# Kernel optimization log

Hardware: AMD Instinct MI355X
Metric: run time of the kernel (lower is better)

The kernel has to match this reference:

```python
import jax, jax.numpy as jnp
import numpy as np

DIM = 1024
NH = 16
HD = DIM // NH  # 64
B, S = 4, 2048
EPS = 1e-5


def layer_norm(x, g, b):
    mu = jnp.mean(x, axis=-1, keepdims=True)
    var = jnp.mean(jnp.square(x - mu), axis=-1, keepdims=True)
    return (x - mu) * jax.lax.rsqrt(var + EPS) * g + b


def setup_inputs() -> dict:
    key = jax.random.key(0)
    ks = jax.random.split(key, 12)
    std = 0.02
    return {
        "x": jax.random.normal(ks[0], (B, S, DIM), jnp.float32),
        "ln1_g": jnp.ones((DIM,), jnp.float32),
        "ln1_b": jnp.zeros((DIM,), jnp.float32),
        # per-head Q/K/V linears stacked over heads: [NH, DIM, HD]
        "Wq": jax.random.normal(ks[1], (NH, DIM, HD), jnp.float32) * std,
        "bq": jnp.zeros((NH, HD), jnp.float32),
        "Wk": jax.random.normal(ks[2], (NH, DIM, HD), jnp.float32) * std,
        "bk": jnp.zeros((NH, HD), jnp.float32),
        "Wv": jax.random.normal(ks[3], (NH, DIM, HD), jnp.float32) * std,
        "bv": jnp.zeros((NH, HD), jnp.float32),
        "ln2_g": jnp.ones((DIM,), jnp.float32),
        "ln2_b": jnp.zeros((DIM,), jnp.float32),
        # FC block: LayerNorm -> Linear(dim,4dim) -> GELU -> Linear(4dim,dim) -> GELU
        "fcln_g": jnp.ones((DIM,), jnp.float32),
        "fcln_b": jnp.zeros((DIM,), jnp.float32),
        "W1": jax.random.normal(ks[4], (DIM, 4 * DIM), jnp.float32) * std,
        "b1": jnp.zeros((4 * DIM,), jnp.float32),
        "W2": jax.random.normal(ks[5], (4 * DIM, DIM), jnp.float32) * std,
        "b2": jnp.zeros((DIM,), jnp.float32),
    }


def reference(x, ln1_g, ln1_b, Wq, bq, Wk, bk, Wv, bv,
              ln2_g, ln2_b, fcln_g, fcln_b, W1, b1, W2, b2):
    # --- MHA branch: x + concat_h(head_h(ln1(x))) ---
    h = layer_norm(x, ln1_g, ln1_b)                       # [B,S,D]
    q = jnp.einsum('bsd,hdk->bhsk', h, Wq) + bq[None, :, None, :]
    k = jnp.einsum('bsd,hdk->bhsk', h, Wk) + bk[None, :, None, :]
    v = jnp.einsum('bsd,hdk->bhsk', h, Wv) + bv[None, :, None, :]
    scores = jnp.einsum('bhsk,bhtk->bhst', q, k) / jnp.sqrt(jnp.float32(HD))
    causal = jnp.tril(jnp.ones((S, S), bool))
    scores = jnp.where(causal[None, None], scores, jnp.float32(-1e9))
    attn = jax.nn.softmax(scores, axis=-1)                # [B,NH,S,S]
    o = jnp.einsum('bhst,bhtk->bhsk', attn, v)            # [B,NH,S,HD]
    o = o.transpose(0, 2, 1, 3).reshape(B, S, DIM)        # concat heads
    x = x + o
    # --- FC branch: x + GELU(GELU(LN(ln2(x)) @ W1) @ W2) ---
    h2 = layer_norm(x, ln2_g, ln2_b)
    h2 = layer_norm(h2, fcln_g, fcln_b)
    h2 = jax.nn.gelu(h2 @ W1 + b1, approximate=False)
    h2 = jax.nn.gelu(h2 @ W2 + b2, approximate=False)
    return x + h2
```

## Files before the change

### kernel.cpp

```cpp
#include <hip/hip_runtime.h>
#include <math.h>

#define DIMD 1024
#define NHD  16
#define HDD  64
#define BBB  4
#define SSS  2048
#define MMM  (BBB*SSS)

typedef __bf16 bf16;
typedef __bf16 bf16x8 __attribute__((ext_vector_type(8)));
typedef __bf16 bf16x4 __attribute__((ext_vector_type(4)));
typedef float  f32x4  __attribute__((ext_vector_type(4)));


__device__ __forceinline__ void gld16(const void* g, void* l) {
  __builtin_amdgcn_global_load_lds((const __attribute__((address_space(1))) void*)g,
                                   (__attribute__((address_space(3))) void*)l,
                                   16, 0, 0);
}

__device__ __forceinline__ f32x4 mfma_bf16(bf16x8 a, bf16x8 b, f32x4 c) {
  return __builtin_amdgcn_mfma_f32_16x16x32_bf16(a, b, c, 0, 0, 0);
}

__device__ __forceinline__ float gelu_f(float x) {
  const float u2 = 1.5957691216057308f * x * (1.0f + 0.044715f * x * x);
  const float e = __expf(u2);
  float r;
  asm("v_rcp_f32 %0, %1" : "=v"(r) : "v"(e + 1.0f));
  return x * (1.0f - r);
}

__device__ __forceinline__ void blockReduce2(float& s, float& s2, float* red) {
  #pragma unroll
  for (int m = 1; m < 64; m <<= 1) {
    s  += __shfl_xor(s,  m);
    s2 += __shfl_xor(s2, m);
  }
  const int wave = threadIdx.x >> 6, lane = threadIdx.x & 63;
  __syncthreads();
  if (lane == 0) { red[wave*2] = s; red[wave*2+1] = s2; }
  __syncthreads();
  s  = red[0] + red[2] + red[4] + red[6];
  s2 = red[1] + red[3] + red[5] + red[7];
}

#define SBAR() do { __builtin_amdgcn_sched_barrier(0); __builtin_amdgcn_s_barrier(); \
                    __builtin_amdgcn_sched_barrier(0); } while (0)
#define LGKM0() do { asm volatile("s_waitcnt lgkmcnt(0)" ::: "memory"); \
                     __builtin_amdgcn_sched_barrier(0); } while (0)
#define LGKMC(n) do { asm volatile("s_waitcnt lgkmcnt(" #n ")" ::: "memory"); \
                      __builtin_amdgcn_sched_barrier(0); } while (0)
#define VMC(n)  do { asm volatile("s_waitcnt vmcnt(" #n ")" ::: "memory"); \
                     __builtin_amdgcn_sched_barrier(0); } while (0)


__global__ __launch_bounds__(256)
void transpose_k(const float* __restrict__ in, bf16* __restrict__ out, int R, int C) {
  __shared__ float tile[32][33];
  const int z = blockIdx.z;
  in  += (size_t)z * R * C;
  out += (size_t)z * R * C;
  const int r0 = blockIdx.x * 32, c0 = blockIdx.y * 32;
  const int tx = threadIdx.x, ty = threadIdx.y;
  #pragma unroll
  for (int k = 0; k < 4; ++k)
    tile[ty + k*8][tx] = in[(size_t)(r0 + ty + k*8) * C + c0 + tx];
  __syncthreads();
  #pragma unroll
  for (int k = 0; k < 4; ++k)
    out[(size_t)(c0 + ty + k*8) * R + r0 + tx] = (bf16)tile[tx][ty + k*8];
}


__global__ __launch_bounds__(256)
void transpose_qkv_k(const float* __restrict__ Wq, const float* __restrict__ Wk,
                     const float* __restrict__ Wv, bf16* __restrict__ out) {
  __shared__ float tile[32][33];
  const int z = blockIdx.z;
  const int which = z >> 4, zh = z & 15;
  const float* in = (which == 0 ? Wq : (which == 1 ? Wk : Wv)) + (size_t)zh * 1024 * 64;
  bf16* op = out + (size_t)z * 64 * 1024;
  const int r0 = blockIdx.x * 32, c0 = blockIdx.y * 32;
  const int tx = threadIdx.x, ty = threadIdx.y;
  #pragma unroll
  for (int k = 0; k < 4; ++k)
    tile[ty + k*8][tx] = in[(size_t)(r0 + ty + k*8) * 64 + c0 + tx];
  __syncthreads();
  #pragma unroll
  for (int k = 0; k < 4; ++k)
    op[(size_t)(c0 + ty + k*8) * 1024 + r0 + tx] = (bf16)tile[tx][ty + k*8];
}


__global__ __launch_bounds__(256)
void transpose_v_k(const bf16* __restrict__ in, bf16* __restrict__ out) {
  __shared__ bf16 t[64*72];
  const int z = blockIdx.y;
  const int s0 = blockIdx.x * 64;
  const bf16* ip = in + (size_t)z * SSS * HDD + (size_t)s0 * HDD;
  bf16* op = out + (size_t)z * SSS * HDD + s0;
  const int tid = threadIdx.x;
  #pragma unroll
  for (int p = 0; p < 2; ++p) {
    const int r = p*32 + (tid >> 3);
    const int c = (tid & 7) * 8;
    const int cs = c ^ (((r >> 3) & 7) << 3);
    *(bf16x8*)&t[r*72 + cs] = *(const bf16x8*)&ip[(size_t)r * HDD + c];
  }
  __syncthreads();
  #pragma unroll
  for (int p = 0; p < 2; ++p) {
    const int hd = p*32 + (tid >> 3);
    const int c0 = (tid & 7) * 8;
    bf16x8 v;
    #pragma unroll
    for (int j = 0; j < 8; ++j) {
      const int r = c0 + j;
      v[j] = t[r*72 + (hd ^ (((r >> 3) & 7) << 3))];
    }
    *(bf16x8*)&op[(size_t)hd * SSS + c0] = v;
  }
}


__global__ __launch_bounds__(256)
void ln1_k(const float* __restrict__ x, const float* __restrict__ g,
           const float* __restrict__ b, bf16* __restrict__ out) {
  __shared__ float red[8];
  const int row = blockIdx.x, t = threadIdx.x;
  const float4 v = ((const float4*)(x + (size_t)row * DIMD))[t];
  float s  = v.x + v.y + v.z + v.w;
  float s2 = v.x*v.x + v.y*v.y + v.z*v.z + v.w*v.w;
  blockReduce2(s, s2, red);
  const float mu   = s * (1.0f / DIMD);
  const float var  = s2 * (1.0f / DIMD) - mu * mu;
  const float rstd = rsqrtf(var + 1e-5f);
  const float4 gv = ((const float4*)g)[t];
  const float4 bv = ((const float4*)b)[t];
  bf16x4 o;
  o[0] = (bf16)((v.x - mu) * rstd * gv.x + bv.x);
  o[1] = (bf16)((v.y - mu) * rstd * gv.y + bv.y);
  o[2] = (bf16)((v.z - mu) * rstd * gv.z + bv.z);
  o[3] = (bf16)((v.w - mu) * rstd * gv.w + bv.w);
  *(bf16x4*)(out + (size_t)row * DIMD + t*4) = o;
}


__global__ __launch_bounds__(256)
void ln2fc_k(const float* __restrict__ x1,
             const float* __restrict__ g2, const float* __restrict__ b2,
             const float* __restrict__ g3, const float* __restrict__ b3,
             bf16* __restrict__ out) {
  __shared__ float red[8];
  const int row = blockIdx.x, t = threadIdx.x;
  const float4 v = ((const float4*)(x1 + (size_t)row * DIMD))[t];
  float s  = v.x + v.y + v.z + v.w;
  float s2 = v.x*v.x + v.y*v.y + v.z*v.z + v.w*v.w;
  blockReduce2(s, s2, red);
  float mu   = s * (1.0f / DIMD);
  float rstd = rsqrtf(s2 * (1.0f / DIMD) - mu * mu + 1e-5f);
  const float4 gv2 = ((const float4*)g2)[t];
  const float4 bv2 = ((const float4*)b2)[t];
  float y0 = (v.x - mu) * rstd * gv2.x + bv2.x;
  float y1 = (v.y - mu) * rstd * gv2.y + bv2.y;
  float y2 = (v.z - mu) * rstd * gv2.z + bv2.z;
  float y3 = (v.w - mu) * rstd * gv2.w + bv2.w;
  s  = y0 + y1 + y2 + y3;
  s2 = y0*y0 + y1*y1 + y2*y2 + y3*y3;
  blockReduce2(s, s2, red);
  mu   = s * (1.0f / DIMD);
  rstd = rsqrtf(s2 * (1.0f / DIMD) - mu * mu + 1e-5f);
  const float4 gv3 = ((const float4*)g3)[t];
  const float4 bv3 = ((const float4*)b3)[t];
  bf16x4 o;
  o[0] = (bf16)((y0 - mu) * rstd * gv3.x + bv3.x);
  o[1] = (bf16)((y1 - mu) * rstd * gv3.y + bv3.y);
  o[2] = (bf16)((y2 - mu) * rstd * gv3.z + bv3.z);
  o[3] = (bf16)((y3 - mu) * rstd * gv3.w + bv3.w);
  *(bf16x4*)(out + (size_t)row * DIMD + t*4) = o;
}


template<int MH2>
__device__ __forceinline__ void load_aH(bf16x8 (&d)[MH2][2], const bf16* base, int roff,
                                        int qv, int sw) {
  #pragma unroll
  for (int mi = 0; mi < MH2; ++mi)
    #pragma unroll
    for (int kk = 0; kk < 2; ++kk)
      d[mi][kk] = *(const bf16x8*)&base[roff + mi*1024 + (((kk<<2)+qv)^sw)*8];
}

__device__ __forceinline__ void load_b2(bf16x8 (&d)[2][2], const bf16* base, int roff,
                                        int qv, int sw) {
  #pragma unroll
  for (int nj = 0; nj < 2; ++nj)
    #pragma unroll
    for (int kk = 0; kk < 2; ++kk)
      d[nj][kk] = *(const bf16x8*)&base[roff + nj*1024 + (((kk<<2)+qv)^sw)*8];
}

template<int EPI, int MH2>
__global__ __launch_bounds__(512)
void gemm8p(const bf16* __restrict__ A, const bf16* __restrict__ Bt,
            int K, int N, int nbx,
            const float* __restrict__ bias, bf16* __restrict__ outB,
            float* __restrict__ outF,
            const float* __restrict__ bq, const float* __restrict__ bk,
            const float* __restrict__ bv) {
  constexpr int BM = 64 * MH2;
  __shared__ bf16 sA[2][BM*64];
  __shared__ bf16 sB[2][256*64];
  const int tid = threadIdx.x, wave = tid >> 6, lane = tid & 63;
  const int wm = wave >> 2, wn = wave & 3;

  const int q8 = gridDim.x >> 3;
  const int wg = (blockIdx.x & 7) * q8 + (blockIdx.x >> 3);
  const int by = wg / nbx, bx = wg - by * nbx;
  const int row0 = by * BM, col0 = bx * 256;

  const int l8 = lane >> 3, l7 = lane & 7;
  const int gsw = (l7 ^ l8) * 8;
  const int lo = lane & 15, qv = lane >> 4, sw = lane & 7;

  const bf16* Ags = A  + (size_t)(row0 + wave*8 + l8) * K + gsw;
  const bf16* Bgs = Bt + (size_t)(col0 + wave*8 + l8) * K + gsw;

  #define STAGE_A(buf, r, kt) gld16(Ags + (size_t)(r)*64*K + (kt), &sA[buf][(r)*4096 + wave*512])
  #define STAGE_B(buf, r, kt) gld16(Bgs + (size_t)(r)*64*K + (kt), &sB[buf][(r)*4096 + wave*512])

  const int fA = (wm*(32*MH2) + lo) * 64;
  const int fB = (wn*64       + lo) * 64;

  f32x4 acc[2*MH2][4] = {};
  bf16x8 aL[MH2][2], aU[MH2][2], b0[2][2], b1[2][2];
  const int NT = K >> 6;

  #pragma unroll
  for (int r = 0; r < MH2; ++r) STAGE_A(0, r, 0);
  #pragma unroll
  for (int r = 0; r < 4; ++r)   STAGE_B(0, r, 0);
  #pragma unroll
  for (int j = 0; j < MH2/2; ++j) STAGE_A(1, 2*j, 64);
  if (MH2 == 4) { VMC(2); } else { VMC(1); }
  SBAR();

  for (int t = 0; t < NT; ++t) {
    const int cur = t & 1, nxt = cur ^ 1;
    const int kt1 = (t + 1) << 6, kt2 = (t + 2) << 6;
    const bf16* cA = &sA[0][0] + cur * (BM*64);
    const bf16* cB = &sB[0][0] + cur * (256*64);

    load_aH<MH2>(aL, cA, fA, qv, sw);
    load_b2(b0, cB, fB, qv, sw);
    load_b2(b1, cB, fB + 2048, qv, sw);
    load_aH<MH2>(aU, cA, fA + MH2*1024, qv, sw);
    if (t + 1 < NT) {
      #pragma unroll
      for (int j = 0; j < MH2/2; ++j) STAGE_A(nxt, 2*j + 1, kt1);
      #pragma unroll
      for (int r = 0; r < 4; ++r)     STAGE_B(nxt, r, kt1);
    }

    if (MH2 == 4) { LGKMC(12); } else { LGKMC(8); }
    __builtin_amdgcn_s_setprio(1);
    #pragma unroll
    for (int mi = 0; mi < MH2; ++mi)
      #pragma unroll
      for (int nj = 0; nj < 2; ++nj)
        #pragma unroll
        for (int kk = 0; kk < 2; ++kk)
          acc[mi][nj] = mfma_bf16(aL[mi][kk], b0[nj][kk], acc[mi][nj]);
    __builtin_amdgcn_s_setprio(0);

    if (MH2 == 4) { LGKMC(8); } else { LGKMC(4); }
    __builtin_amdgcn_s_setprio(1);
    #pragma unroll
    for (int mi = 0; mi < MH2; ++mi)
      #pragma unroll
      for (int nj = 0; nj < 2; ++nj)
        #pragma unroll
        for (int kk = 0; kk < 2; ++kk)
          acc[mi][2+nj] = mfma_bf16(aL[mi][kk], b1[nj][kk], acc[mi][2+nj]);
    __builtin_amdgcn_s_setprio(0);

    LGKM0();
    SBAR();
    if (t + 2 < NT) {
      #pragma unroll
      for (int j = 0; j < MH2/2; ++j) STAGE_A(cur, 2*j, kt2);
    }

    __builtin_amdgcn_s_setprio(1);
    #pragma unroll
    for (int mi = 0; mi < MH2; ++mi)
      #pragma unroll
      for (int nj = 0; nj < 2; ++nj)
        #pragma unroll
        for (int kk = 0; kk < 2; ++kk)
          acc[MH2+mi][nj] = mfma_bf16(aU[mi][kk], b0[nj][kk], acc[MH2+mi][nj]);
    #pragma unroll
    for (int mi = 0; mi < MH2; ++mi)
      #pragma unroll
      for (int nj = 0; nj < 2; ++nj)
        #pragma unroll
        for (int kk = 0; kk < 2; ++kk)
          acc[MH2+mi][2+nj] = mfma_bf16(aU[mi][kk], b1[nj][kk], acc[MH2+mi][2+nj]);
    __builtin_amdgcn_s_setprio(0);

    if (t + 1 < NT) {
      if (t + 2 < NT) { if (MH2 == 4) { VMC(2); } else { VMC(1); } }
      else            { VMC(0); }
      SBAR();
    }
  }
  #undef STAGE_A
  #undef STAGE_B

  #pragma unroll
  for (int mi = 0; mi < 2*MH2; ++mi)
    #pragma unroll
    for (int ni = 0; ni < 4; ++ni)
      #pragma unroll
      for (int i = 0; i < 4; ++i) {
        const int row = row0 + wm*(32*MH2) + mi*16 + qv*4 + i;
        const int col = col0 + wn*64 + ni*16 + lo;
        float v = acc[mi][ni][i];
        if (EPI == 0) {
          const int which = col >> 10, h = (col >> 6) & 15, hd = col & 63;
          const float* bp = (which == 0) ? bq : ((which == 1) ? bk : bv);
          v += bp[h*64 + hd];
          if (which == 0) v *= 0.125f;
          const int b_ = row >> 11, s_ = row & 2047;
          const size_t dst = ((((size_t)which*BBB + b_)*NHD + h)*SSS + s_)*HDD + hd;
          outB[dst] = (bf16)v;
        } else if (EPI == 1) {
          v = gelu_f(v + bias[col]);
          outB[(size_t)row * N + col] = (bf16)v;
        } else {
          v = gelu_f(v + bias[col]);
          outF[(size_t)row * N + col] += v;
        }
      }
}


__global__ __launch_bounds__(256)
void attn_k(const bf16* __restrict__ qkv, const bf16* __restrict__ Vt,
            const float* __restrict__ x, float* __restrict__ out) {
  __shared__ bf16 sK[64*72];
  __shared__ bf16 sVt[80*72];
  __shared__ bf16 sP[128*72];
  const int bh = blockIdx.y;
  const int b = bh >> 4, h = bh & 15;
  const int tid = threadIdx.x, wave = tid >> 6, lane = tid & 63;
  const size_t plane = (size_t)BBB * NHD * SSS * HDD;
  const bf16* Qp  = qkv + ((size_t)b * NHD + h) * SSS * HDD;
  const bf16* Kp  = Qp + plane;
  const bf16* Vtp = Vt + ((size_t)b * NHD + h) * SSS * HDD;

  const int r8 = tid >> 3;
  const int c8 = (tid & 7) * 8;
  const int lo = lane & 15, qv = lane >> 4;

  for (int j = tid; j < 16*72; j += 256) sVt[64*72 + j] = (bf16)1.0f;

  for (int pass = 0; pass < 2; ++pass) {
    const int q0 = (pass == 0 ? (int)blockIdx.x : 15 - (int)blockIdx.x) * 128;

    bf16x8 aq[2][2];
    #pragma unroll
    for (int mi = 0; mi < 2; ++mi)
      #pragma unroll
      for (int kk = 0; kk < 2; ++kk)
        aq[mi][kk] = *(const bf16x8*)&Qp[(size_t)(q0 + wave*32 + mi*16 + lo) * HDD
                                         + kk*32 + qv * 8];

    f32x4 o[2][5] = {};

    bf16x8 rk0, rk1, rv0, rv1;
    rk0 = *(const bf16x8*)&Kp[(size_t)r8 * HDD + c8];
    rk1 = *(const bf16x8*)&Kp[(size_t)(32 + r8) * HDD + c8];
    rv0 = *(const bf16x8*)&Vtp[(size_t)r8 * SSS + c8];
    rv1 = *(const bf16x8*)&Vtp[(size_t)(32 + r8) * SSS + c8];

    const int nt = (q0 + 128) / 64;
    for (int t = 0; t < nt; ++t) {
      const int kv0 = t * 64;
      __syncthreads();
      *(bf16x8*)&sK[r8*72 + c8]        = rk0;
      *(bf16x8*)&sK[(32 + r8)*72 + c8] = rk1;
      *(bf16x8*)&sVt[r8*72 + c8]        = rv0;
      *(bf16x8*)&sVt[(32 + r8)*72 + c8] = rv1;
      __syncthreads();
      if (t + 1 < nt) {
        const int kn = kv0 + 64;
        rk0 = *(const bf16x8*)&Kp[(size_t)(kn + r8) * HDD + c8];
        rk1 = *(const bf16x8*)&Kp[(size_t)(kn + 32 + r8) * HDD + c8];
        rv0 = *(const bf16x8*)&Vtp[(size_t)r8 * SSS + kn + c8];
        rv1 = *(const bf16x8*)&Vtp[(size_t)(32 + r8) * SSS + kn + c8];
      }
      if (kv0 <= q0 + wave*32 + 31) {
        f32x4 s[2][4] = {};
        #pragma unroll
        for (int kk = 0; kk < 2; ++kk)
          #pragma unroll
          for (int ni = 0; ni < 4; ++ni) {
            const bf16x8 ak_ = *(const bf16x8*)&sK[(ni*16 + lo)*72 + kk*32 + qv*8];
            s[0][ni] = mfma_bf16(ak_, aq[0][kk], s[0][ni]);
            s[1][ni] = mfma_bf16(ak_, aq[1][kk], s[1][ni]);
          }
        if (kv0 + 63 > q0 + wave*32) {
          #pragma unroll
          for (int mi = 0; mi < 2; ++mi)
            #pragma unroll
            for (int ni = 0; ni < 4; ++ni)
              #pragma unroll
              for (int i = 0; i < 4; ++i) {
                const int kvg = kv0 + ni*16 + qv*4 + i;
                const int qg  = q0 + wave*32 + mi*16 + lo;
                if (kvg > qg) s[mi][ni][i] = -1e30f;
              }
        }
        #pragma unroll
        for (int mi = 0; mi < 2; ++mi)
          #pragma unroll
          for (int ni = 0; ni < 4; ++ni) {
            bf16x4 pk;
            #pragma unroll
            for (int i = 0; i < 4; ++i) pk[i] = (bf16)__expf(s[mi][ni][i]);
            *(bf16x4*)&sP[(wave*32 + mi*16 + lo)*72 + ni*16 + qv*4] = pk;
          }
        asm volatile("s_waitcnt lgkmcnt(0)" ::: "memory");
        __builtin_amdgcn_sched_barrier(0);
        #pragma unroll
        for (int ks = 0; ks < 2; ++ks) {
          bf16x8 ap[2];
          ap[0] = *(const bf16x8*)&sP[(wave*32 +      lo)*72 + ks*32 + qv*8];
          ap[1] = *(const bf16x8*)&sP[(wave*32 + 16 + lo)*72 + ks*32 + qv*8];
          #pragma unroll
          for (int hf = 0; hf < 5; ++hf) {
            const bf16x8 bv_ = *(const bf16x8*)&sVt[(hf*16 + lo)*72 + ks*32 + qv*8];
            o[0][hf] = mfma_bf16(ap[0], bv_, o[0][hf]);
            o[1][hf] = mfma_bf16(ap[1], bv_, o[1][hf]);
          }
        }
      }
    }
    #pragma unroll
    for (int mi = 0; mi < 2; ++mi) {
      float inv[4];
      #pragma unroll
      for (int i = 0; i < 4; ++i) inv[i] = 1.0f / o[mi][4][i];
      #pragma unroll
      for (int hf = 0; hf < 4; ++hf)
        #pragma unroll
        for (int i = 0; i < 4; ++i) {
          const int srow = q0 + wave*32 + mi*16 + qv*4 + i;
          const int col  = h*HDD + hf*16 + lo;
          const size_t idx = ((size_t)b * SSS + srow) * DIMD + col;
          out[idx] = x[idx] + o[mi][hf][i] * inv[i];
        }
    }
  }
}


extern "C" void kernel_launch(void* const* d_in, const int* in_sizes, int n_in,
                              void* d_out, int out_size, void* d_ws, size_t ws_size,
                              hipStream_t stream) {
  const float* x     = (const float*)d_in[0];
  const float* ln1g  = (const float*)d_in[1];
  const float* ln1b  = (const float*)d_in[2];
  const float* Wq    = (const float*)d_in[3];
  const float* bq    = (const float*)d_in[4];
  const float* Wk    = (const float*)d_in[5];
  const float* bk    = (const float*)d_in[6];
  const float* Wv    = (const float*)d_in[7];
  const float* bv    = (const float*)d_in[8];
  const float* ln2g  = (const float*)d_in[9];
  const float* ln2b  = (const float*)d_in[10];
  const float* fclng = (const float*)d_in[11];
  const float* fclnb = (const float*)d_in[12];
  const float* W1    = (const float*)d_in[13];
  const float* b1    = (const float*)d_in[14];
  const float* W2    = (const float*)d_in[15];
  const float* b2    = (const float*)d_in[16];
  float* out = (float*)d_out;

  char* ws = (char*)d_ws;
  bf16* h     = (bf16*)(ws);
  bf16* Wqkvt = (bf16*)(ws + 16777216);
  bf16* W1t   = (bf16*)(ws + 23068672);
  bf16* W2t   = (bf16*)(ws + 31457280);
  bf16* qkv   = (bf16*)(ws + 39845888);
  bf16* u     = (bf16*)(ws + 39845888);
  bf16* VtB   = h;
  const size_t plane = (size_t)BBB * NHD * SSS * HDD;

  const dim3 tb(32, 8);
  transpose_qkv_k<<<dim3(32, 2, 48), tb, 0, stream>>>(Wq, Wk, Wv, Wqkvt);
  transpose_k<<<dim3(32, 128, 1), tb, 0, stream>>>(W1, W1t, 1024, 4096);
  transpose_k<<<dim3(128, 32, 1), tb, 0, stream>>>(W2, W2t, 4096, 1024);

  ln1_k<<<MMM, 256, 0, stream>>>(x, ln1g, ln1b, h);

  gemm8p<0,2><<<dim3(768), 512, 0, stream>>>(h, Wqkvt, 1024, 3072, 12,
                                             nullptr, qkv, nullptr, bq, bk, bv);

  transpose_v_k<<<dim3(SSS/64, BBB*NHD), 256, 0, stream>>>(qkv + 2*plane, VtB);

  attn_k<<<dim3(8, BBB*NHD), 256, 0, stream>>>(qkv, VtB, x, out);

  ln2fc_k<<<MMM, 256, 0, stream>>>(out, ln2g, ln2b, fclng, fclnb, h);

  gemm8p<1,4><<<dim3(512), 512, 0, stream>>>(h, W1t, 1024, 4096, 16,
                                             b1, u, nullptr, nullptr, nullptr, nullptr);

  gemm8p<2,2><<<dim3(256), 512, 0, stream>>>(u, W2t, 4096, 1024, 4,
                                             b2, nullptr, out, nullptr, nullptr, nullptr);
}
```

Baseline: 339.0 us.

## Restructure GEMM main loop into 8-phase ping-pong schedule with finer-grained staging

Rewrites the gemm8p main loop to process two K-tiles per iteration. Each tile is split into four MFMA quadrants, and each quadrant is separated by barriers, with LDS fragment loads and global-to-LDS staging interleaved between them. B tiles are now prefetched a full stage ahead, and the global loads are spread evenly across phases. The aim is better overlap of memory traffic with MFMA work, at the cost of many more workgroup barriers. The loop also assumes NT is even.

Result: slower. 359.0 us (+5.9%).

```diff
diff --git a/kernel.cpp b/kernel.cpp
--- a/kernel.cpp
+++ b/kernel.cpp
@@ -50,8 +50,6 @@
                     __builtin_amdgcn_sched_barrier(0); } while (0)
 #define LGKM0() do { asm volatile("s_waitcnt lgkmcnt(0)" ::: "memory"); \
                      __builtin_amdgcn_sched_barrier(0); } while (0)
-#define LGKMC(n) do { asm volatile("s_waitcnt lgkmcnt(" #n ")" ::: "memory"); \
-                      __builtin_amdgcn_sched_barrier(0); } while (0)
 #define VMC(n)  do { asm volatile("s_waitcnt vmcnt(" #n ")" ::: "memory"); \
                      __builtin_amdgcn_sched_barrier(0); } while (0)
 
@@ -202,6 +200,20 @@
       d[nj][kk] = *(const bf16x8*)&base[roff + nj*1024 + (((kk<<2)+qv)^sw)*8];
 }
 
+template<int AM, int AN, int MH2>
+__device__ __forceinline__ void quad(f32x4 (&acc)[2*MH2][4], const bf16x8 (&af)[MH2][2],
+                                     const bf16x8 (&bf_)[2][2]) {
+  __builtin_amdgcn_s_setprio(1);
+  #pragma unroll
+  for (int mi = 0; mi < MH2; ++mi)
+    #pragma unroll
+    for (int nj = 0; nj < 2; ++nj)
+      #pragma unroll
+      for (int kk = 0; kk < 2; ++kk)
+        acc[AM+mi][AN+nj] = mfma_bf16(af[mi][kk], bf_[nj][kk], acc[AM+mi][AN+nj]);
+  __builtin_amdgcn_s_setprio(0);
+}
+
 template<int EPI, int MH2>
 __global__ __launch_bounds__(512)
 void gemm8p(const bf16* __restrict__ A, const bf16* __restrict__ Bt,
@@ -237,82 +249,86 @@
   f32x4 acc[2*MH2][4] = {};
   bf16x8 aL[MH2][2], aU[MH2][2], b0[2][2], b1[2][2];
   const int NT = K >> 6;
-
-  #pragma unroll
-  for (int r = 0; r < MH2; ++r) STAGE_A(0, r, 0);
-  #pragma unroll
-  for (int r = 0; r < 4; ++r)   STAGE_B(0, r, 0);
-  #pragma unroll
-  for (int j = 0; j < MH2/2; ++j) STAGE_A(1, 2*j, 64);
-  if (MH2 == 4) { VMC(2); } else { VMC(1); }
+  const int NI = NT >> 1;
+
+  const bf16* cA0 = &sA[0][0];
+  const bf16* cB0 = &sB[0][0];
+  const bf16* cA1 = &sA[1][0];
+  const bf16* cB1 = &sB[1][0];
+
+  if (MH2 == 4) {
+    STAGE_A(0,0,0); STAGE_A(0,1,0); STAGE_A(0,2,0); STAGE_A(0,3,0);
+    STAGE_B(0,0,0); STAGE_B(0,1,0); STAGE_B(0,2,0); STAGE_B(0,3,0);
+    STAGE_A(1,0,64); STAGE_A(1,2,64);
+    STAGE_B(1,0,64); STAGE_B(1,1,64); STAGE_B(1,2,64); STAGE_B(1,3,64);
+    VMC(6);
+  } else {
+    STAGE_A(0,0,0); STAGE_A(0,1,0);
+    STAGE_B(0,0,0); STAGE_B(0,1,0); STAGE_B(0,2,0); STAGE_B(0,3,0);
+    STAGE_B(1,0,64); STAGE_B(1,1,64); STAGE_B(1,2,64); STAGE_B(1,3,64);
+    VMC(4);
+  }
   SBAR();
 
-  for (int t = 0; t < NT; ++t) {
-    const int cur = t & 1, nxt = cur ^ 1;
-    const int kt1 = (t + 1) << 6, kt2 = (t + 2) << 6;
-    const bf16* cA = &sA[0][0] + cur * (BM*64);
-    const bf16* cB = &sB[0][0] + cur * (256*64);
-
-    load_aH<MH2>(aL, cA, fA, qv, sw);
-    load_b2(b0, cB, fB, qv, sw);
-    load_b2(b1, cB, fB + 2048, qv, sw);
-    load_aH<MH2>(aU, cA, fA + MH2*1024, qv, sw);
-    if (t + 1 < NT) {
-      #pragma unroll
-      for (int j = 0; j < MH2/2; ++j) STAGE_A(nxt, 2*j + 1, kt1);
-      #pragma unroll
-      for (int r = 0; r < 4; ++r)     STAGE_B(nxt, r, kt1);
+  for (int i = 0; i < NI; ++i) {
+    const int kb = (2*i + 1) << 6;
+    const int k2 = (2*i + 2) << 6, k3 = (2*i + 3) << 6;
+    const bool more = (i + 1 < NI);
+
+    load_aH<MH2>(aL, cA0, fA, qv, sw);
+    load_b2(b0, cB0, fB, qv, sw);
+    if (MH2 == 4) { STAGE_A(1,1,kb); STAGE_A(1,3,kb); }
+    else          { STAGE_A(1,0,kb); STAGE_A(1,1,kb); }
+    SBAR(); LGKM0();
+    quad<0,0,MH2>(acc, aL, b0);
+    SBAR();
+
+    load_b2(b1, cB0, fB + 2048, qv, sw);
+    if (MH2 == 4 && more) { STAGE_A(0,0,k2); STAGE_A(0,2,k2); }
+    SBAR(); LGKM0();
+    quad<0,2,MH2>(acc, aL, b1);
+    SBAR();
+
+    load_aH<MH2>(aU, cA0, fA + MH2*1024, qv, sw);
+    if (more) { STAGE_B(0,0,k2); STAGE_B(0,1,k2); }
+    SBAR(); LGKM0();
+    quad<MH2,0,MH2>(acc, aU, b0);
+    SBAR();
+
+    if (more) { STAGE_B(0,2,k2); STAGE_B(0,3,k2); }
+    SBAR();
+    quad<MH2,2,MH2>(acc, aU, b1);
+    if (more) { if (MH2 == 4) { VMC(6); } else { VMC(4); } }
+    else      { VMC(0); }
+    SBAR();
+
+    load_aH<MH2>(aL, cA1, fA, qv, sw);
+    load_b2(b0, cB1, fB, qv, sw);
+    if (more) {
+      if (MH2 == 4) { STAGE_A(0,1,k2); STAGE_A(0,3,k2); }
+      else          { STAGE_A(0,0,k2); STAGE_A(0,1,k2); }
     }
-
-    if (MH2 == 4) { LGKMC(12); } else { LGKMC(8); }
-    __builtin_amdgcn_s_setprio(1);
-    #pragma unroll
-    for (int mi = 0; mi < MH2; ++mi)
-      #pragma unroll
-      for (int nj = 0; nj < 2; ++nj)
-        #pragma unroll
-        for (int kk = 0; kk < 2; ++kk)
-          acc[mi][nj] = mfma_bf16(aL[mi][kk], b0[nj][kk], acc[mi][nj]);
-    __builtin_amdgcn_s_setprio(0);
-
-    if (MH2 == 4) { LGKMC(8); } else { LGKMC(4); }
-    __builtin_amdgcn_s_setprio(1);
-    #pragma unroll
-    for (int mi = 0; mi < MH2; ++mi)
-      #pragma unroll
-      for (int nj = 0; nj < 2; ++nj)
-        #pragma unroll
-        for (int kk = 0; kk < 2; ++kk)
-          acc[mi][2+nj] = mfma_bf16(aL[mi][kk], b1[nj][kk], acc[mi][2+nj]);
-    __builtin_amdgcn_s_setprio(0);
-
-    LGKM0();
-    SBAR();
-    if (t + 2 < NT) {
-      #pragma unroll
-      for (int j = 0; j < MH2/2; ++j) STAGE_A(cur, 2*j, kt2);
-    }
-
-    __builtin_amdgcn_s_setprio(1);
-    #pragma unroll
-    for (int mi = 0; mi < MH2; ++mi)
-      #pragma unroll
-      for (int nj = 0; nj < 2; ++nj)
-        #pragma unroll
-        for (int kk = 0; kk < 2; ++kk)
-          acc[MH2+mi][nj] = mfma_bf16(aU[mi][kk], b0[nj][kk], acc[MH2+mi][nj]);
-    #pragma unroll
-    for (int mi = 0; mi < MH2; ++mi)
-      #pragma unroll
-      for (int nj = 0; nj < 2; ++nj)
-        #pragma unroll
-        for (int kk = 0; kk < 2; ++kk)
-          acc[MH2+mi][2+nj] = mfma_bf16(aU[mi][kk], b1[nj][kk], acc[MH2+mi][2+nj]);
-    __builtin_amdgcn_s_setprio(0);
-
-    if (t + 1 < NT) {
-      if (t + 2 < NT) { if (MH2 == 4) { VMC(2); } else { VMC(1); } }
-      else            { VMC(0); }
+    SBAR(); LGKM0();
+    quad<0,0,MH2>(acc, aL, b0);
+    SBAR();
+
+    load_b2(b1, cB1, fB + 2048, qv, sw);
+    if (MH2 == 4 && more) { STAGE_A(1,0,k3); STAGE_A(1,2,k3); }
+    SBAR(); LGKM0();
+    quad<0,2,MH2>(acc, aL, b1);
+    SBAR();
+
+    load_aH<MH2>(aU, cA1, fA + MH2*1024, qv, sw);
+    if (more) { STAGE_B(1,0,k3); STAGE_B(1,1,k3); }
+    SBAR(); LGKM0();
+    quad<MH2,0,MH2>(acc, aU, b0);
+    SBAR();
+
+    if (more) { STAGE_B(1,2,k3); STAGE_B(1,3,k3); }
+    SBAR();
+    quad<MH2,2,MH2>(acc, aU, b1);
+    if (more) {
+      if (MH2 == 4) { VMC(6); } else { VMC(4); }
       SBAR();
     }
   }
```

## Triple-buffer A tiles in MH2=2 GEMM and double-buffer K/V in attention

Applied to the files above, without the earlier changes.

For the MH2=2 GEMM variant, A tiles get a three-slot LDS ring with prefetch two steps ahead. This removes the mid-iteration barrier that was needed before restaging A into the current buffer. The attention kernel double-buffers its K and V^T shared tiles, which drops one __syncthreads per KV step. The cost is more LDS per block, which may lower occupancy, and the attention change relies on a single barrier per iteration to keep the buffers safe.

After: 336.3 us, median of 2. About the same (-0.8%).

```diff
diff --git a/kernel.cpp b/kernel.cpp
--- a/kernel.cpp
+++ b/kernel.cpp
@@ -202,6 +202,20 @@
       d[nj][kk] = *(const bf16x8*)&base[roff + nj*1024 + (((kk<<2)+qv)^sw)*8];
 }
 
+template<int AM, int AN, int MH2>
+__device__ __forceinline__ void quad(f32x4 (&acc)[2*MH2][4], const bf16x8 (&af)[MH2][2],
+                                     const bf16x8 (&bf_)[2][2]) {
+  __builtin_amdgcn_s_setprio(1);
+  #pragma unroll
+  for (int mi = 0; mi < MH2; ++mi)
+    #pragma unroll
+    for (int nj = 0; nj < 2; ++nj)
+      #pragma unroll
+      for (int kk = 0; kk < 2; ++kk)
+        acc[AM+mi][AN+nj] = mfma_bf16(af[mi][kk], bf_[nj][kk], acc[AM+mi][AN+nj]);
+  __builtin_amdgcn_s_setprio(0);
+}
+
 template<int EPI, int MH2>
 __global__ __launch_bounds__(512)
 void gemm8p(const bf16* __restrict__ A, const bf16* __restrict__ Bt,
@@ -211,7 +225,8 @@
             const float* __restrict__ bq, const float* __restrict__ bk,
             const float* __restrict__ bv) {
   constexpr int BM = 64 * MH2;
-  __shared__ bf16 sA[2][BM*64];
+  constexpr int NAB = (MH2 == 2) ? 3 : 2;
+  __shared__ bf16 sA[NAB][BM*64];
   __shared__ bf16 sB[2][256*64];
   const int tid = threadIdx.x, wave = tid >> 6, lane = tid & 63;
   const int wm = wave >> 2, wn = wave & 3;
@@ -238,82 +253,83 @@
   bf16x8 aL[MH2][2], aU[MH2][2], b0[2][2], b1[2][2];
   const int NT = K >> 6;
 
-  #pragma unroll
-  for (int r = 0; r < MH2; ++r) STAGE_A(0, r, 0);
-  #pragma unroll
-  for (int r = 0; r < 4; ++r)   STAGE_B(0, r, 0);
-  #pragma unroll
-  for (int j = 0; j < MH2/2; ++j) STAGE_A(1, 2*j, 64);
-  if (MH2 == 4) { VMC(2); } else { VMC(1); }
-  SBAR();
-
-  for (int t = 0; t < NT; ++t) {
-    const int cur = t & 1, nxt = cur ^ 1;
-    const int kt1 = (t + 1) << 6, kt2 = (t + 2) << 6;
-    const bf16* cA = &sA[0][0] + cur * (BM*64);
-    const bf16* cB = &sB[0][0] + cur * (256*64);
-
-    load_aH<MH2>(aL, cA, fA, qv, sw);
-    load_b2(b0, cB, fB, qv, sw);
-    load_b2(b1, cB, fB + 2048, qv, sw);
-    load_aH<MH2>(aU, cA, fA + MH2*1024, qv, sw);
-    if (t + 1 < NT) {
-      #pragma unroll
-      for (int j = 0; j < MH2/2; ++j) STAGE_A(nxt, 2*j + 1, kt1);
-      #pragma unroll
-      for (int r = 0; r < 4; ++r)     STAGE_B(nxt, r, kt1);
+  if constexpr (MH2 == 2) {
+    STAGE_A(0,0,0); STAGE_A(0,1,0);
+    STAGE_B(0,0,0); STAGE_B(0,1,0); STAGE_B(0,2,0); STAGE_B(0,3,0);
+    STAGE_A(1,0,64); STAGE_A(1,1,64);
+    VMC(2); SBAR();
+
+    int ab = 0;
+    for (int t = 0; t < NT; ++t) {
+      const int bb = t & 1, bn = bb ^ 1;
+      const int an = (ab + 2 >= 3) ? (ab - 1) : (ab + 2);
+      const int kt1 = (t + 1) << 6, kt2 = (t + 2) << 6;
+      const bf16* cA = &sA[ab][0];
+      const bf16* cB = &sB[bb][0];
+
+      load_aH<2>(aL, cA, fA, qv, sw);
+      load_b2(b0, cB, fB, qv, sw);
+      load_b2(b1, cB, fB + 2048, qv, sw);
+      load_aH<2>(aU, cA, fA + 2048, qv, sw);
+      if (t + 1 < NT) { STAGE_B(bn,0,kt1); STAGE_B(bn,1,kt1);
+                        STAGE_B(bn,2,kt1); STAGE_B(bn,3,kt1); }
+      if (t + 2 < NT) { STAGE_A(an,0,kt2); STAGE_A(an,1,kt2); }
+
+      LGKMC(8);
+      quad<0,0,2>(acc, aL, b0);
+      LGKMC(4);
+      quad<0,2,2>(acc, aL, b1);
+      LGKM0();
+      quad<2,0,2>(acc, aU, b0);
+      quad<2,2,2>(acc, aU, b1);
+
+      if (t + 2 < NT)      { VMC(2); SBAR(); }
+      else if (t + 1 < NT) { VMC(0); SBAR(); }
+      ab = (ab + 1 >= 3) ? 0 : ab + 1;
     }
-
-    if (MH2 == 4) { LGKMC(12); } else { LGKMC(8); }
-    __builtin_amdgcn_s_setprio(1);
-    #pragma unroll
-    for (int mi = 0; mi < MH2; ++mi)
-      #pragma unroll
-      for (int nj = 0; nj < 2; ++nj)
-        #pragma unroll
-        for (int kk = 0; kk < 2; ++kk)
-          acc[mi][nj] = mfma_bf16(aL[mi][kk], b0[nj][kk], acc[mi][nj]);
-    __builtin_amdgcn_s_setprio(0);
-
-    if (MH2 == 4) { LGKMC(8); } else { LGKMC(4); }
-    __builtin_amdgcn_s_setprio(1);
-    #pragma unroll
-    for (int mi = 0; mi < MH2; ++mi)
-      #pragma unroll
-      for (int nj = 0; nj < 2; ++nj)
-        #pragma unroll
-        for (int kk = 0; kk < 2; ++kk)
-          acc[mi][2+nj] = mfma_bf16(aL[mi][kk], b1[nj][kk], acc[mi][2+nj]);
-    __builtin_amdgcn_s_setprio(0);
-
-    LGKM0();
-    SBAR();
-    if (t + 2 < NT) {
-      #pragma unroll
-      for (int j = 0; j < MH2/2; ++j) STAGE_A(cur, 2*j, kt2);
-    }
-
-    __builtin_amdgcn_s_setprio(1);
-    #pragma unroll
-    for (int mi = 0; mi < MH2; ++mi)
-      #pragma unroll
-      for (int nj = 0; nj < 2; ++nj)
-        #pragma unroll
-        for (int kk = 0; kk < 2; ++kk)
-          acc[MH2+mi][nj] = mfma_bf16(aU[mi][kk], b0[nj][kk], acc[MH2+mi][nj]);
-    #pragma unroll
-    for (int mi = 0; mi < MH2; ++mi)
-      #pragma unroll
-      for (int nj = 0; nj < 2; ++nj)
-        #pragma unroll
-        for (int kk = 0; kk < 2; ++kk)
-          acc[MH2+mi][2+nj] = mfma_bf16(aU[mi][kk], b1[nj][kk], acc[MH2+mi][2+nj]);
-    __builtin_amdgcn_s_setprio(0);
-
-    if (t + 1 < NT) {
-      if (t + 2 < NT) { if (MH2 == 4) { VMC(2); } else { VMC(1); } }
-      else            { VMC(0); }
+  } else {
+    #pragma unroll
+    for (int r = 0; r < MH2; ++r) STAGE_A(0, r, 0);
+    #pragma unroll
+    for (int r = 0; r < 4; ++r)   STAGE_B(0, r, 0);
+    #pragma unroll
+    for (int j = 0; j < MH2/2; ++j) STAGE_A(1, 2*j, 64);
+    VMC(2); SBAR();
+
+    for (int t = 0; t < NT; ++t) {
+      const int cur = t & 1, nxt = cur ^ 1;
+      const int kt1 = (t + 1) << 6, kt2 = (t + 2) << 6;
+      const bf16* cA = &sA[cur][0];
+      const bf16* cB = &sB[cur][0];
+
+      load_aH<MH2>(aL, cA, fA, qv, sw);
+      load_b2(b0, cB, fB, qv, sw);
+      load_b2(b1, cB, fB + 2048, qv, sw);
+      load_aH<MH2>(aU, cA, fA + MH2*1024, qv, sw);
+      if (t + 1 < NT) {
+        #pragma unroll
+        for (int j = 0; j < MH2/2; ++j) STAGE_A(nxt, 2*j + 1, kt1);
+        #pragma unroll
+        for (int r = 0; r < 4; ++r)     STAGE_B(nxt, r, kt1);
+      }
+
+      LGKMC(12);
+      quad<0,0,MH2>(acc, aL, b0);
+      LGKMC(8);
+      quad<0,2,MH2>(acc, aL, b1);
+      LGKM0();
       SBAR();
+      if (t + 2 < NT) {
+        #pragma unroll
+        for (int j = 0; j < MH2/2; ++j) STAGE_A(cur, 2*j, kt2);
+      }
+      quad<MH2,0,MH2>(acc, aU, b0);
+      quad<MH2,2,MH2>(acc, aU, b1);
+
+      if (t + 1 < NT) {
+        if (t + 2 < NT) { VMC(2); } else { VMC(0); }
+        SBAR();
+      }
     }
   }
   #undef STAGE_A
@@ -350,8 +366,8 @@
 __global__ __launch_bounds__(256)
 void attn_k(const bf16* __restrict__ qkv, const bf16* __restrict__ Vt,
             const float* __restrict__ x, float* __restrict__ out) {
-  __shared__ bf16 sK[64*72];
-  __shared__ bf16 sVt[80*72];
+  __shared__ bf16 sK[2][64*72];
+  __shared__ bf16 sVt[2][80*72];
   __shared__ bf16 sP[128*72];
   const int bh = blockIdx.y;
   const int b = bh >> 4, h = bh & 15;
@@ -365,7 +381,10 @@
   const int c8 = (tid & 7) * 8;
   const int lo = lane & 15, qv = lane >> 4;
 
-  for (int j = tid; j < 16*72; j += 256) sVt[64*72 + j] = (bf16)1.0f;
+  for (int j = tid; j < 16*72; j += 256) {
+    sVt[0][64*72 + j] = (bf16)1.0f;
+    sVt[1][64*72 + j] = (bf16)1.0f;
+  }
 
   for (int pass = 0; pass < 2; ++pass) {
     const int q0 = (pass == 0 ? (int)blockIdx.x : 15 - (int)blockIdx.x) * 128;
@@ -389,11 +408,11 @@
     const int nt = (q0 + 128) / 64;
     for (int t = 0; t < nt; ++t) {
       const int kv0 = t * 64;
-      __syncthreads();
-      *(bf16x8*)&sK[r8*72 + c8]        = rk0;
-      *(bf16x8*)&sK[(32 + r8)*72 + c8] = rk1;
-      *(bf16x8*)&sVt[r8*72 + c8]        = rv0;
-      *(bf16x8*)&sVt[(32 + r8)*72 + c8] = rv1;
+      const int buf = t & 1;
+      *(bf16x8*)&sK[buf][r8*72 + c8]         = rk0;
+      *(bf16x8*)&sK[buf][(32 + r8)*72 + c8]  = rk1;
+      *(bf16x8*)&sVt[buf][r8*72 + c8]        = rv0;
+      *(bf16x8*)&sVt[buf][(32 + r8)*72 + c8] = rv1;
       __syncthreads();
       if (t + 1 < nt) {
         const int kn = kv0 + 64;
@@ -408,7 +427,7 @@
         for (int kk = 0; kk < 2; ++kk)
           #pragma unroll
           for (int ni = 0; ni < 4; ++ni) {
-            const bf16x8 ak_ = *(const bf16x8*)&sK[(ni*16 + lo)*72 + kk*32 + qv*8];
+            const bf16x8 ak_ = *(const bf16x8*)&sK[buf][(ni*16 + lo)*72 + kk*32 + qv*8];
             s[0][ni] = mfma_bf16(ak_, aq[0][kk], s[0][ni]);
             s[1][ni] = mfma_bf16(ak_, aq[1][kk], s[1][ni]);
           }
@@ -442,7 +461,7 @@
           ap[1] = *(const bf16x8*)&sP[(wave*32 + 16 + lo)*72 + ks*32 + qv*8];
           #pragma unroll
           for (int hf = 0; hf < 5; ++hf) {
-            const bf16x8 bv_ = *(const bf16x8*)&sVt[(hf*16 + lo)*72 + ks*32 + qv*8];
+            const bf16x8 bv_ = *(const bf16x8*)&sVt[buf][(hf*16 + lo)*72 + ks*32 + qv*8];
             o[0][hf] = mfma_bf16(ap[0], bv_, o[0][hf]);
             o[1][hf] = mfma_bf16(ap[1], bv_, o[1][hf]);
           }
```
